# Kernel optimization log

Measured on AMD Instinct MI355X. Metric: run time of the kernel, lower is better.

Reference implementation:

```python
import jax, jax.numpy as jnp
import numpy as np

N, DIM, H, D = 8192, 1152, 16, 72
SEGS = 4  # equal-length image segments


def setup_inputs() -> dict:
    key = jax.random.key(0)
    ks = jax.random.split(key, 8)
    s = 0.02
    return {
        "hidden_states": jax.random.normal(ks[0], (N, DIM), jnp.float32),
        "cos": jax.random.uniform(ks[1], (N, D), jnp.float32, -1.0, 1.0),
        "sin": jax.random.uniform(ks[2], (N, D), jnp.float32, -1.0, 1.0),
        "cu_seqlens": (jnp.arange(SEGS + 1, dtype=jnp.int32) * (N // SEGS)),
        "w_qkv": jax.random.normal(ks[3], (DIM, 3 * DIM), jnp.float32) * s,
        "b_qkv": jax.random.normal(ks[4], (3 * DIM,), jnp.float32) * s,
        "w_proj": jax.random.normal(ks[5], (DIM, DIM), jnp.float32) * s,
        "b_proj": jax.random.normal(ks[6], (DIM,), jnp.float32) * s,
    }


def _rope(x, cos, sin):
    # x: [N, H, D]; cos/sin: [N, 1, D]
    half = x.shape[-1] // 2
    x1, x2 = x[..., :half], x[..., half:]
    rot = jnp.concatenate([-x2, x1], axis=-1)
    return x * cos + rot * sin


def reference(hidden_states, cos, sin, cu_seqlens, w_qkv, b_qkv, w_proj, b_proj):
    n = hidden_states.shape[0]
    qkv = (hidden_states @ w_qkv + b_qkv).reshape(n, 3, H, D)
    q, k, v = qkv[:, 0], qkv[:, 1], qkv[:, 2]
    c = cos[:, None, :]
    s = sin[:, None, :]
    q = _rope(q, c, s)
    k = _rope(k, c, s)
    # equal-length segments derived statically from cu_seqlens
    segs = int(cu_seqlens.shape[0]) - 1
    L = n // segs
    qs = q.reshape(segs, L, H, D)
    ks = k.reshape(segs, L, H, D)
    vs = v.reshape(segs, L, H, D)
    scale = D ** -0.5
    scores = jnp.einsum("slhd,smhd->shlm", qs, ks) * scale
    attn = jax.nn.softmax(scores, axis=-1)
    out = jnp.einsum("shlm,smhd->slhd", attn, vs).reshape(n, DIM)
    return out @ w_proj + b_proj
```

## Files before the change

### kernel.cpp

```cpp
#include <hip/hip_runtime.h>
#include <hip/hip_bf16.h>
#include <cstdint>
#include <cstddef>

typedef __bf16 bf16;
typedef __attribute__((ext_vector_type(8))) __bf16 bf16x8;
typedef __attribute__((ext_vector_type(4))) float f32x4;
typedef __attribute__((ext_vector_type(16))) float f32x16;
typedef __attribute__((ext_vector_type(4))) float floatx4;
typedef __attribute__((ext_vector_type(4))) unsigned short ushort4_t;
typedef __attribute__((ext_vector_type(2))) unsigned uint2_t;
typedef __attribute__((ext_vector_type(4))) unsigned uint4_t;

#define NTOK 8192
#define DIMM 1152
#define NH   16
#define HD   72
#define SEGS 4
#define SEGL 2048

__device__ __forceinline__ void gload16(const void* gsrc, void* ldst) {
  __builtin_amdgcn_global_load_lds(
      (const __attribute__((address_space(1))) void*)gsrc,
      (__attribute__((address_space(3))) void*)ldst,
      16, 0, 0);
}

__device__ __forceinline__ unsigned cvtpk(float a, float b) {
  unsigned r;
  asm volatile("v_cvt_pk_bf16_f32 %0, %1, %2" : "=v"(r) : "v"(a), "v"(b));
  return r;
}

__global__ __launch_bounds__(256) void k_cvt(const float* __restrict__ src,
                                             bf16* __restrict__ dst, int n8) {
  int i = blockIdx.x * 256 + threadIdx.x;
  if (i >= n8) return;
  const floatx4* s = (const floatx4*)src + (size_t)i * 2;
  floatx4 a = s[0], b = s[1];
  uint4_t o;
  o[0] = cvtpk(a.x, a.y);
  o[1] = cvtpk(a.z, a.w);
  o[2] = cvtpk(b.x, b.y);
  o[3] = cvtpk(b.z, b.w);
  *((uint4_t*)dst + i) = o;
}

__global__ __launch_bounds__(256) void k_twt(const float* __restrict__ src,
                                             bf16* __restrict__ dst, int R, int C) {
  __shared__ bf16 tile[64][73];
  int bc = blockIdx.x * 64, br = blockIdx.y * 64;
  int t = threadIdx.x;
#pragma unroll
  for (int i = 0; i < 16; i++) {
    int idx = i * 256 + t;
    int r = idx >> 6, c = idx & 63;
    float v = (bc + c < C) ? src[(size_t)(br + r) * C + bc + c] : 0.f;
    tile[c][r] = (bf16)v;
  }
  __syncthreads();
#pragma unroll
  for (int i = 0; i < 16; i++) {
    int idx = i * 256 + t;
    int r = idx >> 6, c = idx & 63;
    dst[(size_t)(bc + r) * R + br + c] = tile[r][c];
  }
}

template <int BM, int BN, int MI, int NI, int THREADS, bool OUT_F32>
__global__ __launch_bounds__(THREADS, 2) void k_gemmP(const bf16* __restrict__ A,
                                                      const bf16* __restrict__ Bt,
                                                      const float* __restrict__ bias,
                                                      void* __restrict__ Cout,
                                                      int M, int Nreal, int K, int gx) {
  __shared__ bf16 sA[3][BM * 32];
  __shared__ bf16 sB[3][BN * 32];
  constexpr int WN = BN / (NI * 16);
  constexpr int nA = (BM * 4) / THREADS;
  constexpr int nB = (BN * 4) / THREADS;
  constexpr int NLD = nA + nB;
  static_assert(NLD == 3 || NLD == 4, "vmcnt literal");
  const int t = threadIdx.x, wave = t >> 6, lane = t & 63;
  const int lr = lane & 15, lg = lane >> 4;
  const int nwg = gridDim.x, bid = blockIdx.x;
  const int swz = (bid & 7) * (nwg >> 3) + (bid >> 3);
  const int bx = swz % gx, by = swz / gx;
  const int m0 = by * BM, n0 = bx * BN;
  const int wr = wave / WN, wc = wave % WN;
  const int NS = K >> 5;

  f32x4 acc[MI][NI];
#pragma unroll
  for (int i = 0; i < MI; i++)
#pragma unroll
    for (int j = 0; j < NI; j++)
#pragma unroll
      for (int q = 0; q < 4; q++) acc[i][j][q] = 0.f;

  const bf16* Ab = A + (size_t)m0 * K;
  const bf16* Bb = Bt + (size_t)n0 * K;
  const int glsw = ((t & 3) ^ ((t >> 3) & 3)) * 8;
  const int rbase = t >> 2;

  auto STAGE = [&](int slot, int k0) {
#pragma unroll
    for (int p = 0; p < nA; ++p)
      gload16(Ab + (size_t)(rbase + p * (THREADS / 4)) * K + k0 + glsw,
              (char*)&sA[slot][0] + p * (THREADS * 16) + wave * 1024);
#pragma unroll
    for (int p = 0; p < nB; ++p)
      gload16(Bb + (size_t)(rbase + p * (THREADS / 4)) * K + k0 + glsw,
              (char*)&sB[slot][0] + p * (THREADS * 16) + wave * 1024);
  };

  const int swz4 = (lr >> 1) & 3;
  const int aoff = (wr * MI * 16 + lr) * 32 + ((lg ^ swz4) * 8);
  const int boff = (wc * NI * 16 + lr) * 32 + ((lg ^ swz4) * 8);

  STAGE(0, 0);
  STAGE(1, 32);

  int slot = 0;
  for (int j = 0; j < NS; ++j) {
    if (j == NS - 1) {
      asm volatile("s_waitcnt vmcnt(0)" ::: "memory");
    } else if constexpr (NLD == 3) {
      asm volatile("s_waitcnt vmcnt(3)" ::: "memory");
    } else {
      asm volatile("s_waitcnt vmcnt(4)" ::: "memory");
    }
    __builtin_amdgcn_s_barrier();
    __builtin_amdgcn_sched_barrier(0);
    bf16x8 av[MI], bv[NI];
#pragma unroll
    for (int mi = 0; mi < MI; mi++)
      av[mi] = *(const bf16x8*)&sA[slot][aoff + mi * 512];
#pragma unroll
    for (int ni = 0; ni < NI; ni++)
      bv[ni] = *(const bf16x8*)&sB[slot][boff + ni * 512];
    asm volatile("s_waitcnt lgkmcnt(0)" ::: "memory");
    __builtin_amdgcn_sched_barrier(0);
    if (j + 2 < NS) {
      int s2 = slot + 2; if (s2 >= 3) s2 -= 3;
      STAGE(s2, (j + 2) * 32);
    }
    __builtin_amdgcn_s_setprio(1);
#pragma unroll
    for (int mi = 0; mi < MI; mi++)
#pragma unroll
      for (int ni = 0; ni < NI; ni++)
        acc[mi][ni] = __builtin_amdgcn_mfma_f32_16x16x32_bf16(av[mi], bv[ni], acc[mi][ni], 0, 0, 0);
    __builtin_amdgcn_s_setprio(0);
    if (++slot == 3) slot = 0;
  }

#pragma unroll
  for (int mi = 0; mi < MI; ++mi)
#pragma unroll
    for (int ni = 0; ni < NI; ++ni) {
      int col = n0 + wc * NI * 16 + ni * 16 + lr;
      if (col < Nreal) {
        float bc_ = bias[col];
#pragma unroll
        for (int j = 0; j < 4; j++) {
          int row = m0 + wr * MI * 16 + mi * 16 + lg * 4 + j;
          float v = acc[mi][ni][j] + bc_;
          if (OUT_F32)
            ((float*)Cout)[(size_t)row * Nreal + col] = v;
          else
            ((bf16*)Cout)[(size_t)row * Nreal + col] = (bf16)v;
        }
      }
    }
}

__global__ __launch_bounds__(256) void k_rope(const bf16* __restrict__ qkv,
                                              const float* __restrict__ cs,
                                              const float* __restrict__ sn,
                                              bf16* __restrict__ Qp,
                                              bf16* __restrict__ Kp) {
  int n = blockIdx.x;
  int s = n >> 11, l = n & 2047;
  const bf16* row = qkv + (size_t)n * (3 * DIMM);
  const float* cr = cs + (size_t)n * HD;
  const float* sr = sn + (size_t)n * HD;
  const float QS = 0.17002323f;
  for (int e = threadIdx.x; e < 3072; e += 256) {
    int which = e / 1536;
    int r = e - which * 1536;
    int h = r / 96;
    int d = r - h * 96;
    float v = 0.f;
    if (d < HD) {
      int base = which * DIMM + h * HD;
      float x = (float)row[base + d];
      float o = (d < 36) ? -(float)row[base + d + 36] : (float)row[base + d - 36];
      v = x * cr[d] + o * sr[d];
      if (which == 0) v *= QS;
    }
    bf16* dst = which ? Kp : Qp;
    dst[(((size_t)(s * NH + h) * 3 + (d >> 5)) * SEGL + l) * 32 + (d & 31)] = (bf16)v;
  }
}

__global__ __launch_bounds__(256) void k_vrep(const bf16* __restrict__ qkv,
                                              bf16* __restrict__ Vt) {
  int s = blockIdx.z, h = blockIdx.y, l0 = blockIdx.x * 64;
  __shared__ bf16 tl[64][73];
  int t = threadIdx.x;
  for (int idx = t; idx < 64 * HD; idx += 256) {
    int l = idx / HD, d = idx - l * HD;
    tl[l][d] = qkv[(size_t)(s * SEGL + l0 + l) * (3 * DIMM) + 2 * DIMM + h * HD + d];
  }
  __syncthreads();
  for (int idx = t; idx < 96 * 64; idx += 256) {
    int d = idx >> 6, l = idx & 63;
    bf16 v = (d < HD) ? tl[l][d] : ((d == HD) ? (bf16)1.f : (bf16)0.f);
    Vt[((size_t)(s * NH + h) * 96 + d) * SEGL + l0 + l] = v;
  }
}

__global__ __launch_bounds__(256, 2) void k_attn(const bf16* __restrict__ Qg,
                                                 const bf16* __restrict__ Kg,
                                                 const bf16* __restrict__ Vg,
                                                 bf16* __restrict__ Oo) {
  __shared__ bf16 sK[2][3 * 64 * 32];
  __shared__ bf16 sV[2][96 * 64];
  const int t = threadIdx.x, wave = t >> 6, lane = t & 63;
  const int c = lane & 31, hi = lane >> 5;
  const int bid = blockIdx.x;
  const int g = ((bid >> 6) << 3) | (bid & 7);
  const int qt = (bid >> 3) & 7;
  const int s = g >> 4, h = g & 15, q0 = qt * 256;
  const bf16* Qb = Qg + (size_t)(s * NH + h) * 3 * SEGL * 32;
  const bf16* Kb = Kg + (size_t)(s * NH + h) * 3 * SEGL * 32;
  const bf16* Vb = Vg + (size_t)(s * NH + h) * 96 * SEGL;

  const bf16* kq[3];
  const bf16* vq[3];
#pragma unroll
  for (int i = 0; i < 3; i++) {
    int ch = wave * 3 + i;
    int kk = ch >> 2;
    int r = (ch & 3) * 16 + (lane >> 2);
    int gg = (lane & 3) ^ ((r >> 1) & 3);
    kq[i] = Kb + (size_t)kk * (SEGL * 32) + (size_t)r * 32 + gg * 8;
    int rv = ch * 8 + (lane >> 3);
    int gv = (lane & 7) ^ (rv & 7);
    vq[i] = Vb + (size_t)rv * SEGL + gv * 8;
  }

  bf16x8 Qf[2][5];
#pragma unroll
  for (int sni = 0; sni < 2; sni++)
#pragma unroll
    for (int kk = 0; kk < 5; kk++) {
      int qr = q0 + wave * 64 + sni * 32 + c;
      Qf[sni][kk] = *(const bf16x8*)&Qb[(size_t)(kk >> 1) * (SEGL * 32) +
                                        (size_t)qr * 32 + ((kk & 1) * 2 + hi) * 8];
    }

#pragma unroll
  for (int i = 0; i < 3; i++) {
    gload16(kq[i], (char*)sK[0] + (wave * 3 + i) * 1024);
    gload16(vq[i], (char*)sV[0] + (wave * 3 + i) * 1024);
    kq[i] += 2048;
    vq[i] += 64;
  }
  __syncthreads();

  f32x16 accO[3][2];
#pragma unroll
  for (int df = 0; df < 3; df++)
#pragma unroll
    for (int sni = 0; sni < 2; sni++)
#pragma unroll
      for (int r = 0; r < 16; r++) accO[df][sni][r] = 0.f;
  f32x16 ZC;
#pragma unroll
  for (int r = 0; r < 16; r++) ZC[r] = 0.f;

  int cur = 0;
  for (int tile = 0; tile < 32; ++tile) {
    if (tile + 1 < 32) {
#pragma unroll
      for (int i = 0; i < 3; i++) {
        gload16(kq[i], (char*)sK[cur ^ 1] + (wave * 3 + i) * 1024);
        gload16(vq[i], (char*)sV[cur ^ 1] + (wave * 3 + i) * 1024);
        kq[i] += 2048;
        vq[i] += 64;
      }
    }

    f32x16 S[2][2];
    __builtin_amdgcn_s_setprio(1);
#pragma unroll
    for (int kk = 0; kk < 5; kk++) {
      bf16x8 Kf[2];
#pragma unroll
      for (int smi = 0; smi < 2; smi++) {
        int kr = smi * 32 + c;
        int gg = (((kk & 1) * 2 + hi) ^ ((kr >> 1) & 3));
        Kf[smi] = *(const bf16x8*)&sK[cur][(kk >> 1) * 2048 + kr * 32 + gg * 8];
      }
#pragma unroll
      for (int smi = 0; smi < 2; smi++)
#pragma unroll
        for (int sni = 0; sni < 2; sni++)
          S[smi][sni] = __builtin_amdgcn_mfma_f32_32x32x16_bf16(
              Kf[smi], Qf[sni][kk], kk ? S[smi][sni] : ZC, 0, 0, 0);
    }
    __builtin_amdgcn_s_setprio(0);

    __builtin_amdgcn_s_setprio(1);
#pragma unroll
    for (int kk = 0; kk < 4; kk++) {
      bf16x8 Vf[3];
#pragma unroll
      for (int df = 0; df < 3; df++) {
        int dr = df * 32 + c;
        int gg = ((kk * 2 + hi) ^ (dr & 7));
        Vf[df] = *(const bf16x8*)&sV[cur][dr * 64 + gg * 8];
      }
#pragma unroll
      for (int sni = 0; sni < 2; sni++) {
        const int smi = kk >> 1;
        const int base = (kk & 1) * 8;
        unsigned u0 = cvtpk(__builtin_amdgcn_exp2f(S[smi][sni][base + 0]),
                            __builtin_amdgcn_exp2f(S[smi][sni][base + 1]));
        unsigned u1 = cvtpk(__builtin_amdgcn_exp2f(S[smi][sni][base + 2]),
                            __builtin_amdgcn_exp2f(S[smi][sni][base + 3]));
        unsigned u2 = cvtpk(__builtin_amdgcn_exp2f(S[smi][sni][base + 4]),
                            __builtin_amdgcn_exp2f(S[smi][sni][base + 5]));
        unsigned u3 = cvtpk(__builtin_amdgcn_exp2f(S[smi][sni][base + 6]),
                            __builtin_amdgcn_exp2f(S[smi][sni][base + 7]));
        asm volatile("v_permlane32_swap_b32 %0, %1" : "+v"(u0), "+v"(u2));
        asm volatile("v_permlane32_swap_b32 %0, %1" : "+v"(u1), "+v"(u3));
        union { bf16x8 v; unsigned u[4]; } pb;
        pb.u[0] = u0; pb.u[1] = u1; pb.u[2] = u2; pb.u[3] = u3;
#pragma unroll
        for (int df = 0; df < 3; df++)
          accO[df][sni] = __builtin_amdgcn_mfma_f32_32x32x16_bf16(Vf[df], pb.v, accO[df][sni], 0, 0, 0);
      }
    }
    __builtin_amdgcn_s_setprio(0);

    __syncthreads();
    cur ^= 1;
  }

#pragma unroll
  for (int sni = 0; sni < 2; sni++) {
    float lown = accO[2][sni][4];
    float lv = lown + __shfl_xor(lown, 32, 64);
    float inv = 1.f / lv;
    int token = s * SEGL + q0 + wave * 64 + sni * 32 + c;
#pragma unroll
    for (int df = 0; df < 3; df++)
#pragma unroll
      for (int rg = 0; rg < 4; rg++) {
        int d0 = df * 32 + rg * 8 + hi * 4;
        if (d0 < HD) {
          uint2_t w;
          w[0] = cvtpk(accO[df][sni][rg * 4 + 0] * inv, accO[df][sni][rg * 4 + 1] * inv);
          w[1] = cvtpk(accO[df][sni][rg * 4 + 2] * inv, accO[df][sni][rg * 4 + 3] * inv);
          *(uint2_t*)&Oo[(size_t)token * DIMM + h * HD + d0] = w;
        }
      }
  }
}

extern "C" void kernel_launch(void* const* d_in, const int* in_sizes, int n_in,
                              void* d_out, int out_size, void* d_ws, size_t ws_size,
                              hipStream_t stream) {
  (void)in_sizes; (void)n_in; (void)out_size; (void)ws_size;
  const float* hs     = (const float*)d_in[0];
  const float* cosp   = (const float*)d_in[1];
  const float* sinp   = (const float*)d_in[2];
  const float* w_qkv  = (const float*)d_in[4];
  const float* b_qkv  = (const float*)d_in[5];
  const float* w_proj = (const float*)d_in[6];
  const float* b_proj = (const float*)d_in[7];
  float* out = (float*)d_out;

  char* ws = (char*)d_ws;
  bf16* hsb    = (bf16*)(ws + 0);
  bf16* wprojT = (bf16*)(ws + 26836992);
  bf16* qkv    = (bf16*)(ws + 29491200);
  bf16* Qp     = (bf16*)(ws + 86114304);
  bf16* Kp     = (bf16*)(ws + 111280128);
  bf16* Vt     = (bf16*)(ws + 136445952);
  bf16* ao     = (bf16*)(ws + 161611776);
  bf16* wqkvT  = (bf16*)(ws + 161611776);

  k_cvt<<<4608, 256, 0, stream>>>(hs, hsb, 1179648);
  k_twt<<<dim3(56, 18), 256, 0, stream>>>(w_qkv, wqkvT, 1152, 3456);
  k_twt<<<dim3(18, 18), 256, 0, stream>>>(w_proj, wprojT, 1152, 1152);
  k_gemmP<128, 256, 4, 4, 512, false><<<896, 512, 0, stream>>>(
      hsb, wqkvT, b_qkv, (void*)qkv, 8192, 3456, 1152, 14);
  k_rope<<<8192, 256, 0, stream>>>(qkv, cosp, sinp, Qp, Kp);
  k_vrep<<<dim3(32, 16, 4), 256, 0, stream>>>(qkv, Vt);
  k_attn<<<512, 256, 0, stream>>>(Qp, Kp, Vt, ao);
  k_gemmP<128, 128, 4, 4, 256, true><<<576, 256, 0, stream>>>(
      ao, wprojT, b_proj, (void*)out, 8192, 1152, 1152, 9);
}
```

Measured before the change: 289.8 us.

## Merge prep and RoPE/V kernels, add 256x256 QKV GEMM, vectorize RoPE

Fuses the three preprocessing launches (activation convert and two weight transposes) into one kernel, and fuses RoPE with the V repack into another, which cuts launch count and tail effects. Replaces the QKV projection GEMM with a new 256x256-tile, double-buffered kernel that uses swizzled LDS and setprio around the MFMA block. RoPE is rewritten to process 8 elements per thread with vector loads and packed bf16 stores. The output GEMM's occupancy hint is raised to 3 waves per SIMD, which may constrain registers. The larger GEMM tiles raise LDS and register use and leave fewer blocks to fill the machine.

```diff
diff --git a/kernel.cpp b/kernel.cpp
--- a/kernel.cpp
+++ b/kernel.cpp
@@ -4,11 +4,11 @@
 #include <cstddef>
 
 typedef __bf16 bf16;
+typedef __attribute__((ext_vector_type(4))) __bf16 bf16x4;
 typedef __attribute__((ext_vector_type(8))) __bf16 bf16x8;
 typedef __attribute__((ext_vector_type(4))) float f32x4;
 typedef __attribute__((ext_vector_type(16))) float f32x16;
 typedef __attribute__((ext_vector_type(4))) float floatx4;
-typedef __attribute__((ext_vector_type(4))) unsigned short ushort4_t;
 typedef __attribute__((ext_vector_type(2))) unsigned uint2_t;
 typedef __attribute__((ext_vector_type(4))) unsigned uint4_t;
 
@@ -32,25 +32,35 @@
   return r;
 }
 
-__global__ __launch_bounds__(256) void k_cvt(const float* __restrict__ src,
-                                             bf16* __restrict__ dst, int n8) {
-  int i = blockIdx.x * 256 + threadIdx.x;
-  if (i >= n8) return;
-  const floatx4* s = (const floatx4*)src + (size_t)i * 2;
-  floatx4 a = s[0], b = s[1];
-  uint4_t o;
-  o[0] = cvtpk(a.x, a.y);
-  o[1] = cvtpk(a.z, a.w);
-  o[2] = cvtpk(b.x, b.y);
-  o[3] = cvtpk(b.z, b.w);
-  *((uint4_t*)dst + i) = o;
-}
-
-__global__ __launch_bounds__(256) void k_twt(const float* __restrict__ src,
-                                             bf16* __restrict__ dst, int R, int C) {
+__global__ __launch_bounds__(256) void k_prep(const float* __restrict__ hs,
+                                              bf16* __restrict__ hsb,
+                                              const float* __restrict__ wq,
+                                              bf16* __restrict__ wqT,
+                                              const float* __restrict__ wp,
+                                              bf16* __restrict__ wpT) {
   __shared__ bf16 tile[64][73];
-  int bc = blockIdx.x * 64, br = blockIdx.y * 64;
-  int t = threadIdx.x;
+  const int b = blockIdx.x, t = threadIdx.x;
+  if (b < 4608) {
+    int i = b * 256 + t;
+    const floatx4* s = (const floatx4*)hs + (size_t)i * 2;
+    floatx4 a = s[0], c = s[1];
+    uint4_t o;
+    o[0] = cvtpk(a.x, a.y);
+    o[1] = cvtpk(a.z, a.w);
+    o[2] = cvtpk(c.x, c.y);
+    o[3] = cvtpk(c.z, c.w);
+    *((uint4_t*)hsb + i) = o;
+    return;
+  }
+  const float* src; bf16* dst; int R, C, bx, by;
+  if (b < 4608 + 1008) {
+    int idx = b - 4608;
+    src = wq; dst = wqT; R = 1152; C = 3456; bx = idx % 56; by = idx / 56;
+  } else {
+    int idx = b - 5616;
+    src = wp; dst = wpT; R = 1152; C = 1152; bx = idx % 18; by = idx / 18;
+  }
+  int bc = bx * 64, br = by * 64;
 #pragma unroll
   for (int i = 0; i < 16; i++) {
     int idx = i * 256 + t;
@@ -67,8 +77,116 @@
   }
 }
 
+template <bool OUT_F32>
+__global__ __launch_bounds__(512, 2) void k_gemm8(const bf16* __restrict__ A,
+                                                  const bf16* __restrict__ Bt,
+                                                  const float* __restrict__ bias,
+                                                  void* __restrict__ Cout,
+                                                  int M, int Nreal, int K, int gx) {
+  __shared__ bf16 sA[2][2][256 * 32];
+  __shared__ bf16 sB[2][2][256 * 32];
+  const int t = threadIdx.x, wave = t >> 6, lane = t & 63;
+  const int lr = lane & 15, lg = lane >> 4;
+  const int nwg = gridDim.x, bid = blockIdx.x;
+  const int swz = (bid & 7) * (nwg >> 3) + (bid >> 3);
+  const int bx = swz % gx, by = swz / gx;
+  const int m0 = by * 256, n0 = bx * 256;
+  const int wr = wave >> 2;
+  const int wn = (wave & 3) * 64;
+  const int NT = K >> 6;
+
+  f32x4 acc[8][4];
+#pragma unroll
+  for (int i = 0; i < 8; i++)
+#pragma unroll
+    for (int j = 0; j < 4; j++)
+#pragma unroll
+      for (int q = 0; q < 4; q++) acc[i][j][q] = 0.f;
+
+  const bf16* Ab = A + (size_t)m0 * K;
+  const bf16* Bb = Bt + (size_t)n0 * K;
+  const int glsw = ((t & 3) ^ ((t >> 3) & 3)) * 8;
+  const bf16* Asrc0 = Ab + (size_t)(t >> 2) * K + glsw;
+  const bf16* Asrc1 = Ab + (size_t)((t >> 2) + 128) * K + glsw;
+  const bf16* Bsrc0 = Bb + (size_t)(t >> 2) * K + glsw;
+  const bf16* Bsrc1 = Bb + (size_t)((t >> 2) + 128) * K + glsw;
+  const int swz4 = (lr >> 1) & 3;
+  const int aoff = (wr * 128 + lr) * 32 + ((lg ^ swz4) * 8);
+  const int boff = (wn + lr) * 32 + ((lg ^ swz4) * 8);
+
+#pragma unroll
+  for (int kh = 0; kh < 2; ++kh) {
+    const int k0 = kh * 32;
+    char* dA = (char*)&sA[0][kh][0] + wave * 1024;
+    char* dB = (char*)&sB[0][kh][0] + wave * 1024;
+    gload16(Asrc0 + k0, dA);
+    gload16(Bsrc0 + k0, dB);
+    gload16(Asrc1 + k0, dA + 8192);
+    gload16(Bsrc1 + k0, dB + 8192);
+  }
+
+  for (int kt = 0; kt < NT; ++kt) {
+    const int buf = kt & 1;
+    const bool more = (kt + 1 < NT);
+#pragma unroll
+    for (int kh = 0; kh < 2; ++kh) {
+      if (!more && kh == 1) {
+        asm volatile("s_waitcnt vmcnt(0)" ::: "memory");
+      } else {
+        asm volatile("s_waitcnt vmcnt(4)" ::: "memory");
+      }
+      __builtin_amdgcn_s_barrier();
+      __builtin_amdgcn_sched_barrier(0);
+      const bf16* As = &sA[buf][kh][0];
+      const bf16* Bs = &sB[buf][kh][0];
+      bf16x8 av[8], bv[4];
+#pragma unroll
+      for (int mi = 0; mi < 8; mi++)
+        av[mi] = *(const bf16x8*)&As[aoff + mi * 512];
+#pragma unroll
+      for (int ni = 0; ni < 4; ni++)
+        bv[ni] = *(const bf16x8*)&Bs[boff + ni * 512];
+      if (more) {
+        const int k0 = (kt + 1) * 64 + kh * 32;
+        char* dA = (char*)&sA[buf ^ 1][kh][0] + wave * 1024;
+        char* dB = (char*)&sB[buf ^ 1][kh][0] + wave * 1024;
+        gload16(Asrc0 + k0, dA);
+        gload16(Bsrc0 + k0, dB);
+        gload16(Asrc1 + k0, dA + 8192);
+        gload16(Bsrc1 + k0, dB + 8192);
+      }
+      __builtin_amdgcn_s_setprio(1);
+#pragma unroll
+      for (int mi = 0; mi < 8; mi++)
+#pragma unroll
+        for (int ni = 0; ni < 4; ni++)
+          acc[mi][ni] = __builtin_amdgcn_mfma_f32_16x16x32_bf16(av[mi], bv[ni], acc[mi][ni], 0, 0, 0);
+      __builtin_amdgcn_s_setprio(0);
+    }
+  }
+
+#pragma unroll
+  for (int mi = 0; mi < 8; ++mi)
+#pragma unroll
+    for (int ni = 0; ni < 4; ++ni) {
+      int col = n0 + wn + ni * 16 + lr;
+      if (col < Nreal) {
+        float bc_ = bias[col];
+#pragma unroll
+        for (int j = 0; j < 4; j++) {
+          int row = m0 + wr * 128 + mi * 16 + lg * 4 + j;
+          float v = acc[mi][ni][j] + bc_;
+          if (OUT_F32)
+            ((float*)Cout)[(size_t)row * Nreal + col] = v;
+          else
+            ((bf16*)Cout)[(size_t)row * Nreal + col] = (bf16)v;
+        }
+      }
+    }
+}
+
 template <int BM, int BN, int MI, int NI, int THREADS, bool OUT_F32>
-__global__ __launch_bounds__(THREADS, 2) void k_gemmP(const bf16* __restrict__ A,
+__global__ __launch_bounds__(THREADS, 3) void k_gemmP(const bf16* __restrict__ A,
                                                       const bf16* __restrict__ Bt,
                                                       const float* __restrict__ bias,
                                                       void* __restrict__ Cout,
@@ -174,49 +292,88 @@
     }
 }
 
-__global__ __launch_bounds__(256) void k_rope(const bf16* __restrict__ qkv,
-                                              const float* __restrict__ cs,
-                                              const float* __restrict__ sn,
-                                              bf16* __restrict__ Qp,
-                                              bf16* __restrict__ Kp) {
-  int n = blockIdx.x;
-  int s = n >> 11, l = n & 2047;
-  const bf16* row = qkv + (size_t)n * (3 * DIMM);
-  const float* cr = cs + (size_t)n * HD;
-  const float* sr = sn + (size_t)n * HD;
-  const float QS = 0.17002323f;
-  for (int e = threadIdx.x; e < 3072; e += 256) {
-    int which = e / 1536;
-    int r = e - which * 1536;
-    int h = r / 96;
-    int d = r - h * 96;
-    float v = 0.f;
-    if (d < HD) {
-      int base = which * DIMM + h * HD;
-      float x = (float)row[base + d];
-      float o = (d < 36) ? -(float)row[base + d + 36] : (float)row[base + d - 36];
-      v = x * cr[d] + o * sr[d];
-      if (which == 0) v *= QS;
-    }
-    bf16* dst = which ? Kp : Qp;
-    dst[(((size_t)(s * NH + h) * 3 + (d >> 5)) * SEGL + l) * 32 + (d & 31)] = (bf16)v;
-  }
-}
-
-__global__ __launch_bounds__(256) void k_vrep(const bf16* __restrict__ qkv,
-                                              bf16* __restrict__ Vt) {
-  int s = blockIdx.z, h = blockIdx.y, l0 = blockIdx.x * 64;
-  __shared__ bf16 tl[64][73];
-  int t = threadIdx.x;
-  for (int idx = t; idx < 64 * HD; idx += 256) {
-    int l = idx / HD, d = idx - l * HD;
-    tl[l][d] = qkv[(size_t)(s * SEGL + l0 + l) * (3 * DIMM) + 2 * DIMM + h * HD + d];
-  }
-  __syncthreads();
-  for (int idx = t; idx < 96 * 64; idx += 256) {
-    int d = idx >> 6, l = idx & 63;
-    bf16 v = (d < HD) ? tl[l][d] : ((d == HD) ? (bf16)1.f : (bf16)0.f);
-    Vt[((size_t)(s * NH + h) * 96 + d) * SEGL + l0 + l] = v;
+__global__ __launch_bounds__(256) void k_ropev(const bf16* __restrict__ qkv,
+                                               const float* __restrict__ cs,
+                                               const float* __restrict__ sn,
+                                               bf16* __restrict__ Qp,
+                                               bf16* __restrict__ Kp,
+                                               bf16* __restrict__ Vt) {
+  __shared__ bf16 tl[64][80];
+  const int bid = blockIdx.x, t = threadIdx.x;
+  if (bid < 2048) {
+    const float QS = 0.17002323f;
+    const int n0 = bid * 4;
+#pragma unroll
+    for (int it = 0; it < 6; ++it) {
+      int idx = it * 256 + t;
+      int tok = idx / 384;
+      int r = idx - tok * 384;
+      int which = r / 192;
+      int r2 = r - which * 192;
+      int h = r2 / 12;
+      int d0 = (r2 - h * 12) * 8;
+      int n = n0 + tok;
+      bf16* dst = which ? Kp : Qp;
+      size_t ob = ((((size_t)((n >> 11) * NH + h)) * 3 + (d0 >> 5)) * SEGL +
+                   (n & 2047)) * 32 + (d0 & 31);
+      if (d0 >= HD) {
+        uint4_t z = {0u, 0u, 0u, 0u};
+        *(uint4_t*)&dst[ob] = z;
+        continue;
+      }
+      const bf16* rowp = qkv + (size_t)n * (3 * DIMM) + which * DIMM + h * HD;
+      bf16x8 xv = *(const bf16x8*)&rowp[d0];
+      float ov[8];
+      if (d0 == 32) {
+        bf16x4 a = *(const bf16x4*)&rowp[68];
+        bf16x4 b = *(const bf16x4*)&rowp[0];
+#pragma unroll
+        for (int j = 0; j < 4; j++) { ov[j] = -(float)a[j]; ov[j + 4] = (float)b[j]; }
+      } else if (d0 < 32) {
+        bf16x4 a = *(const bf16x4*)&rowp[d0 + 36];
+        bf16x4 b = *(const bf16x4*)&rowp[d0 + 40];
+#pragma unroll
+        for (int j = 0; j < 4; j++) { ov[j] = -(float)a[j]; ov[j + 4] = -(float)b[j]; }
+      } else {
+        bf16x4 a = *(const bf16x4*)&rowp[d0 - 36];
+        bf16x4 b = *(const bf16x4*)&rowp[d0 - 32];
+#pragma unroll
+        for (int j = 0; j < 4; j++) { ov[j] = (float)a[j]; ov[j + 4] = (float)b[j]; }
+      }
+      const float* cr = cs + (size_t)n * HD + d0;
+      const float* sr = sn + (size_t)n * HD + d0;
+      floatx4 c0 = *(const floatx4*)cr, c1 = *(const floatx4*)(cr + 4);
+      floatx4 s0 = *(const floatx4*)sr, s1 = *(const floatx4*)(sr + 4);
+      float vv[8];
+#pragma unroll
+      for (int j = 0; j < 4; j++) {
+        vv[j] = (float)xv[j] * c0[j] + ov[j] * s0[j];
+        vv[j + 4] = (float)xv[j + 4] * c1[j] + ov[j + 4] * s1[j];
+      }
+      if (!which) {
+#pragma unroll
+        for (int j = 0; j < 8; j++) vv[j] *= QS;
+      }
+      uint4_t w;
+      w[0] = cvtpk(vv[0], vv[1]);
+      w[1] = cvtpk(vv[2], vv[3]);
+      w[2] = cvtpk(vv[4], vv[5]);
+      w[3] = cvtpk(vv[6], vv[7]);
+      *(uint4_t*)&dst[ob] = w;
+    }
+  } else {
+    int idx2 = bid - 2048;
+    int s = idx2 >> 9, h = (idx2 >> 5) & 15, l0 = (idx2 & 31) * 64;
+    for (int idx = t; idx < 64 * HD; idx += 256) {
+      int l = idx / HD, d = idx - l * HD;
+      tl[l][d] = qkv[(size_t)(s * SEGL + l0 + l) * (3 * DIMM) + 2 * DIMM + h * HD + d];
+    }
+    __syncthreads();
+    for (int idx = t; idx < 96 * 64; idx += 256) {
+      int d = idx >> 6, l = idx & 63;
+      bf16 v = (d < HD) ? tl[l][d] : ((d == HD) ? (bf16)1.f : (bf16)0.f);
+      Vt[((size_t)(s * NH + h) * 96 + d) * SEGL + l0 + l] = v;
+    }
   }
 }
 
@@ -393,13 +550,9 @@
   bf16* ao     = (bf16*)(ws + 161611776);
   bf16* wqkvT  = (bf16*)(ws + 161611776);
 
-  k_cvt<<<4608, 256, 0, stream>>>(hs, hsb, 1179648);
-  k_twt<<<dim3(56, 18), 256, 0, stream>>>(w_qkv, wqkvT, 1152, 3456);
-  k_twt<<<dim3(18, 18), 256, 0, stream>>>(w_proj, wprojT, 1152, 1152);
-  k_gemmP<128, 256, 4, 4, 512, false><<<896, 512, 0, stream>>>(
-      hsb, wqkvT, b_qkv, (void*)qkv, 8192, 3456, 1152, 14);
-  k_rope<<<8192, 256, 0, stream>>>(qkv, cosp, sinp, Qp, Kp);
-  k_vrep<<<dim3(32, 16, 4), 256, 0, stream>>>(qkv, Vt);
+  k_prep<<<5940, 256, 0, stream>>>(hs, hsb, w_qkv, wqkvT, w_proj, wprojT);
+  k_gemm8<false><<<448, 512, 0, stream>>>(hsb, wqkvT, b_qkv, (void*)qkv, 8192, 3456, 1152, 14);
+  k_ropev<<<4096, 256, 0, stream>>>(qkv, cosp, sinp, Qp, Kp, Vt);
   k_attn<<<512, 256, 0, stream>>>(Qp, Kp, Vt, ao);
   k_gemmP<128, 128, 4, 4, 256, true><<<576, 256, 0, stream>>>(
       ao, wprojT, b_proj, (void*)out, 8192, 1152, 1152, 9);
```

New measurement: 244.1 us (median of 3 runs). -15.8%, faster.
